# Performance work log

Measured on AMD Instinct MI355X. Metric: run time of the kernel, lower is better.

Reference implementation:

```python
import jax, jax.numpy as jnp
import numpy as np


def setup_inputs() -> dict:
    key = jax.random.key(0)
    k1, k2 = jax.random.split(key)
    N, D = 8192, 256
    cond_feature = jax.random.normal(k1, (N, D), dtype=jnp.float32)
    sol_feature = jax.random.normal(k2, (N, D), dtype=jnp.float32)
    temperature = jnp.asarray(0.5, dtype=jnp.float32)  # learned scalar, used as exp(temperature)
    return {"cond_feature": cond_feature, "sol_feature": sol_feature, "temperature": temperature}


def reference(cond_feature, sol_feature, temperature):
    N = cond_feature.shape[0]
    c = cond_feature.reshape(N, -1)  # [N, D]
    s = sol_feature.reshape(sol_feature.shape[0], -1)  # [N, D]
    # pairwise L2 distance via ||a||^2 + ||b||^2 - 2 a.b (avoids N x N x D intermediate)
    c2 = jnp.sum(c * c, axis=-1)  # [N]
    s2 = jnp.sum(s * s, axis=-1)  # [N]
    d2 = c2[:, None] + s2[None, :] - 2.0 * jnp.einsum('nd,md->nm', c, s)
    dist = jnp.sqrt(jnp.maximum(d2, 0.0))  # [N, N]
    sim = -dist * jnp.exp(temperature)
    # cross_entropy(sim, arange) + cross_entropy(sim.T, arange): diagonal of log-softmax both ways
    logp_row = jax.nn.log_softmax(sim, axis=-1)  # CE over rows
    logp_col = jax.nn.log_softmax(sim, axis=0)   # CE over columns == CE(sim.T, labels)
    diag = jnp.arange(N)
    loss_row = -jnp.mean(logp_row[diag, diag])
    loss_col = -jnp.mean(logp_col[diag, diag])
    return (loss_row + loss_col) * 0.5
```

## Files before the change

kernel.cpp:

```cpp
#include <hip/hip_runtime.h>
#include <math.h>

#define DIM 256
#define TM 128
#define TN 128

typedef int   v4i    __attribute__((ext_vector_type(4)));
typedef int   v8i    __attribute__((ext_vector_type(8)));
typedef float f32x16 __attribute__((ext_vector_type(16)));

__global__ __launch_bounds__(256) void convert_kernel(
        const float* __restrict__ C, const float* __restrict__ S,
        unsigned char* __restrict__ Cb, unsigned char* __restrict__ Sb,
        float* __restrict__ c2, float* __restrict__ s2,
        float* __restrict__ ddot, float* __restrict__ sums0,
        float* __restrict__ out, int N) {
    int gtid = blockIdx.x * 256 + threadIdx.x;
    if (gtid < 2 * N) sums0[gtid] = 0.0f;
    if (gtid == 0) out[0] = 0.0f;
    int row = gtid >> 6;
    int l = gtid & 63;
    if (row >= N) return;
    float4 v  = ((const float4*)(C + (size_t)row * DIM))[l];
    float4 sv = ((const float4*)(S + (size_t)row * DIM))[l];
    int pc = __builtin_amdgcn_cvt_pk_fp8_f32(v.x, v.y, 0, false);
    pc     = __builtin_amdgcn_cvt_pk_fp8_f32(v.z, v.w, pc, true);
    int ps = __builtin_amdgcn_cvt_pk_fp8_f32(sv.x, sv.y, 0, false);
    ps     = __builtin_amdgcn_cvt_pk_fp8_f32(sv.z, sv.w, ps, true);
    int idx4 = (row >> 5) * 2048 + (l >> 4) * 512 + ((l >> 2) & 1) * 256
             + ((row & 31) + 32 * ((l >> 3) & 1)) * 4 + (l & 3);
    ((int*)Cb)[idx4] = pc;
    ((int*)Sb)[idx4] = ps;
    float nc = v.x * v.x + v.y * v.y + v.z * v.z + v.w * v.w;
    float ns = sv.x * sv.x + sv.y * sv.y + sv.z * sv.z + sv.w * sv.w;
    float cr = v.x * sv.x + v.y * sv.y + v.z * sv.z + v.w * sv.w;
    #pragma unroll
    for (int off = 32; off > 0; off >>= 1) {
        nc += __shfl_down(nc, off, 64);
        ns += __shfl_down(ns, off, 64);
        cr += __shfl_down(cr, off, 64);
    }
    if (l == 0) { c2[row] = nc; s2[row] = ns; ddot[row] = cr; }
}

__global__ __launch_bounds__(256, 4) void mfma_kernel(
        const unsigned char* __restrict__ Cb, const unsigned char* __restrict__ Sb,
        const float* __restrict__ c2, const float* __restrict__ s2,
        const float* __restrict__ temp,
        float* __restrict__ rowsum, float* __restrict__ colsum, int N) {
    __shared__ float rs[TM], cs[TN], c2t[TM], s2t[TN];

    const int tid = threadIdx.x;
    const int b = blockIdx.x;
    const int xcd = b & 7;
    const int sidx = b >> 3;
    const int bm = (xcd * 8 + (sidx & 7)) * TM;
    const int bn = (sidx >> 3) * TN;

    const int w  = tid >> 6;
    const int l  = tid & 63;
    const int wm = (w >> 1) * 64;
    const int wn = (w & 1) * 64;

    const float escale = __expf(temp[0]);
    const float Kf = escale * 1.4426950408889634f;
    const float K2 = Kf * Kf;
    const float m2K2 = -2.0f * K2;

    if (tid < TM) { rs[tid] = 0.0f; c2t[tid] = K2 * c2[bm + tid]; }
    else { int t = tid - TM; cs[t] = 0.0f; s2t[t] = K2 * s2[bn + t]; }

    const unsigned char* baseA = Cb + (size_t)((bm + wm) >> 5) * 8192 + l * 16;
    const unsigned char* baseB = Sb + (size_t)((bn + wn) >> 5) * 8192 + l * 16;

    f32x16 acc[2][2] = {};

    #pragma unroll
    for (int kk = 0; kk < 4; ++kk) {
        v8i af[2], bf[2];
        #pragma unroll
        for (int t = 0; t < 2; ++t) {
            v4i alo = *(const v4i*)(baseA + t * 8192 + kk * 2048);
            v4i ahi = *(const v4i*)(baseA + t * 8192 + kk * 2048 + 1024);
            af[t] = __builtin_shufflevector(alo, ahi, 0, 1, 2, 3, 4, 5, 6, 7);
            v4i blo = *(const v4i*)(baseB + t * 8192 + kk * 2048);
            v4i bhi = *(const v4i*)(baseB + t * 8192 + kk * 2048 + 1024);
            bf[t] = __builtin_shufflevector(blo, bhi, 0, 1, 2, 3, 4, 5, 6, 7);
        }
        #pragma unroll
        for (int mi = 0; mi < 2; ++mi)
            #pragma unroll
            for (int ni = 0; ni < 2; ++ni)
                acc[mi][ni] = __builtin_amdgcn_mfma_scale_f32_32x32x64_f8f6f4(
                    af[mi], bf[ni], acc[mi][ni], 0, 0,
                    0, 0x7F, 0, 0x7F);
    }

    __syncthreads();

    const int q2 = l >> 5;
    const int col5 = l & 31;
    float s2v[2] = { s2t[wn + col5], s2t[wn + 32 + col5] };

    float rfold[2];
    float cp[2] = {0.f, 0.f};

    #pragma unroll
    for (int mi = 0; mi < 2; ++mi) {
        float c2r[16];
        #pragma unroll
        for (int s = 0; s < 16; ++s)
            c2r[s] = c2t[wm + mi * 32 + (s & 3) + 8 * (s >> 2) + 4 * q2];
        float rp[16];
        #pragma unroll
        for (int s = 0; s < 16; ++s) rp[s] = 0.0f;
        #pragma unroll
        for (int ni = 0; ni < 2; ++ni) {
            #pragma unroll
            for (int s = 0; s < 16; ++s) {
                float d2 = fmaf(m2K2, acc[mi][ni][s], c2r[s] + s2v[ni]);
                d2 = fmaxf(d2, 0.0f);
                float e = __builtin_amdgcn_exp2f(-__builtin_amdgcn_sqrtf(d2));
                rp[s] += e;
                cp[ni] += e;
            }
        }
        #pragma unroll
        for (int bb = 0; bb < 4; ++bb) {
            const int n = 16 >> bb;
            const int bit = (l >> bb) & 1;
            #pragma unroll
            for (int k = 0; k < 8; ++k) {
                if (k < (n >> 1)) {
                    float keep = bit ? rp[2 * k + 1] : rp[2 * k];
                    float send = bit ? rp[2 * k] : rp[2 * k + 1];
                    rp[k] = keep + __shfl_xor(send, 1 << bb, 64);
                }
            }
        }
        rfold[mi] = rp[0];
    }
    const int mymi = (l >> 4) & 1;
    {
        float keep = mymi ? rfold[1] : rfold[0];
        float send = mymi ? rfold[0] : rfold[1];
        float rfin = keep + __shfl_xor(send, 16, 64);
        const int s = l & 15;
        const int myrow = wm + mymi * 32 + (s & 3) + 8 * (s >> 2) + 4 * q2;
        atomicAdd(&rs[myrow], rfin);
    }
    {
        float keep = q2 ? cp[1] : cp[0];
        float send = q2 ? cp[0] : cp[1];
        float cfin = keep + __shfl_xor(send, 32, 64);
        atomicAdd(&cs[wn + q2 * 32 + col5], cfin);
    }

    __syncthreads();
    if (tid < TM) atomicAdd(&rowsum[bm + tid], rs[tid]);
    else atomicAdd(&colsum[bn + tid - TM], cs[tid - TM]);
}

__global__ __launch_bounds__(256) void finalize_kernel(
        const float* __restrict__ rowsum, const float* __restrict__ colsum,
        const float* __restrict__ c2, const float* __restrict__ s2,
        const float* __restrict__ ddot, const float* __restrict__ temp,
        float* __restrict__ out, int N) {
    __shared__ float red[4];
    const float escale = __expf(temp[0]);
    const int tid = threadIdx.x;
    int i = blockIdx.x * 256 + tid;
    float sum = 0.0f;
    if (i < N) {
        float d2 = c2[i] + s2[i] - 2.0f * ddot[i];
        float dist = __builtin_amdgcn_sqrtf(fmaxf(d2, 0.0f));
        sum = __logf(rowsum[i]) + __logf(colsum[i]) + 2.0f * escale * dist;
    }
    #pragma unroll
    for (int off = 32; off > 0; off >>= 1) sum += __shfl_down(sum, off, 64);
    if ((tid & 63) == 0) red[tid >> 6] = sum;
    __syncthreads();
    if (tid == 0)
        atomicAdd(out, (red[0] + red[1] + red[2] + red[3]) / (2.0f * (float)N));
}

extern "C" void kernel_launch(void* const* d_in, const int* in_sizes, int n_in,
                              void* d_out, int out_size, void* d_ws, size_t ws_size,
                              hipStream_t stream) {
    const float* C = (const float*)d_in[0];
    const float* S = (const float*)d_in[1];
    const float* T = (const float*)d_in[2];
    const int N = in_sizes[0] / DIM;

    float* ws     = (float*)d_ws;
    float* c2     = ws;
    float* s2     = ws + N;
    float* rowsum = ws + 2 * N;
    float* colsum = ws + 3 * N;
    float* ddot   = ws + 4 * N;
    unsigned char* Cb = (unsigned char*)(ws + 5 * N + 64);
    unsigned char* Sb = Cb + (size_t)N * DIM;

    convert_kernel<<<(N * 64) / 256, 256, 0, stream>>>(
        C, S, Cb, Sb, c2, s2, ddot, rowsum, (float*)d_out, N);

    mfma_kernel<<<(N / TM) * (N / TN), 256, 0, stream>>>(
        Cb, Sb, c2, s2, T, rowsum, colsum, N);

    finalize_kernel<<<(N + 255) / 256, 256, 0, stream>>>(
        rowsum, colsum, c2, s2, ddot, T, (float*)d_out, N);
}
```

Before: 106.1 us.

## Quantize features to FP4 e2m1 and use FP4 MFMA with plain 2D grid

Operands are now encoded as 4-bit e2m1 values with a threshold-based encoder instead of FP8. The packed layout is halved to match, and the scaled MFMA runs in FP4 mode with zero-padded 16-byte fragments. This is meant to cut operand bytes loaded per tile and raise matrix-op throughput. The XCD-aware block swizzle is also replaced with a plain 2D grid. FP4 without block scaling greatly coarsens the dot products, which risks loss accuracy, and the pairwise epilogue work is unchanged.

```diff
diff --git a/kernel.cpp b/kernel.cpp
--- a/kernel.cpp
+++ b/kernel.cpp
@@ -9,9 +9,19 @@
 typedef int   v8i    __attribute__((ext_vector_type(8)));
 typedef float f32x16 __attribute__((ext_vector_type(16)));
 
+__device__ __forceinline__ unsigned int fp4_enc(float x) {
+    float a = fabsf(x);
+    unsigned int c =
+        (a >= 0.25f ? 1u : 0u) + (a >= 0.75f ? 1u : 0u) +
+        (a >= 1.25f ? 1u : 0u) + (a >= 1.75f ? 1u : 0u) +
+        (a >= 2.5f  ? 1u : 0u) + (a >= 3.5f  ? 1u : 0u) +
+        (a >= 5.0f  ? 1u : 0u);
+    return c | (x < 0.0f ? 8u : 0u);
+}
+
 __global__ __launch_bounds__(256) void convert_kernel(
         const float* __restrict__ C, const float* __restrict__ S,
-        unsigned char* __restrict__ Cb, unsigned char* __restrict__ Sb,
+        unsigned short* __restrict__ Cb, unsigned short* __restrict__ Sb,
         float* __restrict__ c2, float* __restrict__ s2,
         float* __restrict__ ddot, float* __restrict__ sums0,
         float* __restrict__ out, int N) {
@@ -23,14 +33,14 @@
     if (row >= N) return;
     float4 v  = ((const float4*)(C + (size_t)row * DIM))[l];
     float4 sv = ((const float4*)(S + (size_t)row * DIM))[l];
-    int pc = __builtin_amdgcn_cvt_pk_fp8_f32(v.x, v.y, 0, false);
-    pc     = __builtin_amdgcn_cvt_pk_fp8_f32(v.z, v.w, pc, true);
-    int ps = __builtin_amdgcn_cvt_pk_fp8_f32(sv.x, sv.y, 0, false);
-    ps     = __builtin_amdgcn_cvt_pk_fp8_f32(sv.z, sv.w, ps, true);
-    int idx4 = (row >> 5) * 2048 + (l >> 4) * 512 + ((l >> 2) & 1) * 256
-             + ((row & 31) + 32 * ((l >> 3) & 1)) * 4 + (l & 3);
-    ((int*)Cb)[idx4] = pc;
-    ((int*)Sb)[idx4] = ps;
+    unsigned int uc = fp4_enc(v.x) | (fp4_enc(v.y) << 4)
+                    | (fp4_enc(v.z) << 8) | (fp4_enc(v.w) << 12);
+    unsigned int us = fp4_enc(sv.x) | (fp4_enc(sv.y) << 4)
+                    | (fp4_enc(sv.z) << 8) | (fp4_enc(sv.w) << 12);
+    int idx2 = (row >> 5) * 2048 + (l >> 4) * 512
+             + ((row & 31) + 32 * ((l >> 3) & 1)) * 8 + (l & 7);
+    Cb[idx2] = (unsigned short)uc;
+    Sb[idx2] = (unsigned short)us;
     float nc = v.x * v.x + v.y * v.y + v.z * v.z + v.w * v.w;
     float ns = sv.x * sv.x + sv.y * sv.y + sv.z * sv.z + sv.w * sv.w;
     float cr = v.x * sv.x + v.y * sv.y + v.z * sv.z + v.w * sv.w;
@@ -51,12 +61,8 @@
     __shared__ float rs[TM], cs[TN], c2t[TM], s2t[TN];
 
     const int tid = threadIdx.x;
-    const int b = blockIdx.x;
-    const int xcd = b & 7;
-    const int sidx = b >> 3;
-    const int bm = (xcd * 8 + (sidx & 7)) * TM;
-    const int bn = (sidx >> 3) * TN;
-
+    const int bm = blockIdx.y * TM;
+    const int bn = blockIdx.x * TN;
     const int w  = tid >> 6;
     const int l  = tid & 63;
     const int wm = (w >> 1) * 64;
@@ -70,29 +76,28 @@
     if (tid < TM) { rs[tid] = 0.0f; c2t[tid] = K2 * c2[bm + tid]; }
     else { int t = tid - TM; cs[t] = 0.0f; s2t[t] = K2 * s2[bn + t]; }
 
-    const unsigned char* baseA = Cb + (size_t)((bm + wm) >> 5) * 8192 + l * 16;
-    const unsigned char* baseB = Sb + (size_t)((bn + wn) >> 5) * 8192 + l * 16;
+    const unsigned char* baseA = Cb + (size_t)((bm + wm) >> 5) * 4096 + l * 16;
+    const unsigned char* baseB = Sb + (size_t)((bn + wn) >> 5) * 4096 + l * 16;
 
     f32x16 acc[2][2] = {};
+    const v4i z4 = {0, 0, 0, 0};
 
     #pragma unroll
     for (int kk = 0; kk < 4; ++kk) {
         v8i af[2], bf[2];
         #pragma unroll
         for (int t = 0; t < 2; ++t) {
-            v4i alo = *(const v4i*)(baseA + t * 8192 + kk * 2048);
-            v4i ahi = *(const v4i*)(baseA + t * 8192 + kk * 2048 + 1024);
-            af[t] = __builtin_shufflevector(alo, ahi, 0, 1, 2, 3, 4, 5, 6, 7);
-            v4i blo = *(const v4i*)(baseB + t * 8192 + kk * 2048);
-            v4i bhi = *(const v4i*)(baseB + t * 8192 + kk * 2048 + 1024);
-            bf[t] = __builtin_shufflevector(blo, bhi, 0, 1, 2, 3, 4, 5, 6, 7);
+            v4i a4 = *(const v4i*)(baseA + t * 4096 + kk * 1024);
+            v4i b4 = *(const v4i*)(baseB + t * 4096 + kk * 1024);
+            af[t] = __builtin_shufflevector(a4, z4, 0, 1, 2, 3, 4, 5, 6, 7);
+            bf[t] = __builtin_shufflevector(b4, z4, 0, 1, 2, 3, 4, 5, 6, 7);
         }
         #pragma unroll
         for (int mi = 0; mi < 2; ++mi)
             #pragma unroll
             for (int ni = 0; ni < 2; ++ni)
                 acc[mi][ni] = __builtin_amdgcn_mfma_scale_f32_32x32x64_f8f6f4(
-                    af[mi], bf[ni], acc[mi][ni], 0, 0,
+                    af[mi], bf[ni], acc[mi][ni], 4, 4,
                     0, 0x7F, 0, 0x7F);
     }
 
@@ -198,14 +203,16 @@
     float* rowsum = ws + 2 * N;
     float* colsum = ws + 3 * N;
     float* ddot   = ws + 4 * N;
-    unsigned char* Cb = (unsigned char*)(ws + 5 * N + 64);
-    unsigned char* Sb = Cb + (size_t)N * DIM;
+    unsigned short* Cb = (unsigned short*)(ws + 5 * N + 64);
+    unsigned short* Sb = Cb + (size_t)N * DIM / 4;
 
     convert_kernel<<<(N * 64) / 256, 256, 0, stream>>>(
         C, S, Cb, Sb, c2, s2, ddot, rowsum, (float*)d_out, N);
 
-    mfma_kernel<<<(N / TM) * (N / TN), 256, 0, stream>>>(
-        Cb, Sb, c2, s2, T, rowsum, colsum, N);
+    dim3 grid(N / TN, N / TM);
+    mfma_kernel<<<grid, 256, 0, stream>>>(
+        (const unsigned char*)Cb, (const unsigned char*)Sb,
+        c2, s2, T, rowsum, colsum, N);
 
     finalize_kernel<<<(N + 255) / 256, 256, 0, stream>>>(
         rowsum, colsum, c2, s2, ddot, T, (float*)d_out, N);
```

Result: faster. 103.2 us (-2.7%).
